# Kernel optimization log

Measured on AMD Instinct MI355X. Metric: run time of the kernel, lower is better.

## Reference

```python
import jax, jax.numpy as jnp
import numpy as np

B, N, C = 8, 3136, 128
NUM_HEADS = 2
HEAD_DIM = C // NUM_HEADS  # 64
SCALE = HEAD_DIM ** -0.5


def setup_inputs() -> dict:
    key = jax.random.key(0)
    ks = jax.random.split(key, 10)
    s = 0.02
    return {
        "x": jax.random.normal(ks[0], (B, N, C), jnp.float32),
        "H": 56,
        "W": 56,
        "relative_pos": jax.random.normal(ks[1], (NUM_HEADS, N, N), jnp.float32),
        "Wq": jax.random.normal(ks[2], (C, C), jnp.float32) * s,
        "bq": jnp.zeros((C,), jnp.float32),
        "Wk": jax.random.normal(ks[3], (C, C), jnp.float32) * s,
        "bk": jnp.zeros((C,), jnp.float32),
        "Wv": jax.random.normal(ks[4], (C, C), jnp.float32) * s,
        "bv": jnp.zeros((C,), jnp.float32),
        "Wp": jax.random.normal(ks[5], (C, C), jnp.float32) * s,
        "bp": jnp.zeros((C,), jnp.float32),
    }


def reference(x, H, W, relative_pos, Wq, bq, Wk, bk, Wv, bv, Wp, bp):
    # x: [B, N, C]; sr_ratio == 1 path of Attention.forward
    b, n, c = x.shape
    h, dh = NUM_HEADS, HEAD_DIM
    # q/k/v projections -> [B, h, N, dh] (torch Linear: x @ W.T + b)
    q = (x @ Wq.T + bq).reshape(b, n, h, dh).transpose(0, 2, 1, 3)
    k = (x @ Wk.T + bk).reshape(b, n, h, dh).transpose(0, 2, 1, 3)
    v = (x @ Wv.T + bv).reshape(b, n, h, dh).transpose(0, 2, 1, 3)
    # scores with additive relative-position bias: [B, h, N, N]
    attn = jnp.einsum("bhnd,bhmd->bhnm", q, k) * SCALE + relative_pos[None]
    attn = jax.nn.softmax(attn, axis=-1)
    # AV -> [B, N, C]
    out = jnp.einsum("bhnm,bhmd->bhnd", attn, v).transpose(0, 2, 1, 3).reshape(b, n, c)
    return out @ Wp.T + bp
```

## Files before the change

### kernel.cpp

```cpp
#include <hip/hip_runtime.h>
#include <hip/hip_fp16.h>

#define N_TOK 3136
#define DH 64
#define NHEAD 2
#define CDIM 128
#define BATCH 8
#define NT 49
#define QK_SCALE 0.18033688011112f
#define LOG2E 1.4426950408889634f

typedef __attribute__((ext_vector_type(8))) short bf16x8;
typedef __attribute__((ext_vector_type(8))) _Float16 f16x8;
typedef __attribute__((ext_vector_type(2))) _Float16 f16x2;
typedef __attribute__((ext_vector_type(2))) __fp16 fp16x2;
typedef __attribute__((ext_vector_type(4))) float f32x4;
typedef __attribute__((ext_vector_type(16))) float f32x16;
typedef __attribute__((ext_vector_type(4))) unsigned short u16x4;
typedef __attribute__((ext_vector_type(4))) unsigned int u32x4;

__device__ __forceinline__ unsigned short f2bf(float f) {
  unsigned int u = __float_as_uint(f);
  u += 0x7fffu + ((u >> 16) & 1u);
  return (unsigned short)(u >> 16);
}

#define MFMA16(a, b, c)    __builtin_amdgcn_mfma_f32_16x16x32_bf16(a, b, c, 0, 0, 0)
#define MFMA32_BF(a, b, c) __builtin_amdgcn_mfma_f32_32x32x16_bf16(a, b, c, 0, 0, 0)
#define MFMA32_F16(a, b, c) __builtin_amdgcn_mfma_f32_32x32x16_f16(a, b, c, 0, 0, 0)

__device__ __forceinline__ void plswap(unsigned& a, unsigned& b) {
  asm volatile("v_permlane32_swap_b32 %0, %1" : "+v"(a), "+v"(b));
}

__device__ __forceinline__ f16x2 pkrtz(float a, float b) {
  union { fp16x2 p; f16x2 h; } cv;
  cv.p = __builtin_amdgcn_cvt_pkrtz(a, b);
  return cv.h;
}

template<bool IN_F32, int OMODE>
__global__ __launch_bounds__(256)
void proj_gemm(const void* __restrict__ Ain, const float* __restrict__ W,
               const float* __restrict__ bias, void* __restrict__ Out,
               float out_scale)
{
  __shared__ __align__(16) unsigned short xs[64][136];
  __shared__ __align__(16) unsigned short wsh[128][136];
  const int tid = threadIdx.x;
  const int m0 = blockIdx.x * 64;
  const int w = tid >> 6, l = tid & 63;
  const int lk = l & 15, lg = l >> 4;

  {
    const float4* Wv = (const float4*)W;
#pragma unroll
    for (int i = 0; i < 16; ++i) {
      int f = tid + i * 256;
      float4 v = Wv[f];
      int row = f >> 5, col = (f & 31) << 2;
      u16x4 pk = { f2bf(v.x), f2bf(v.y), f2bf(v.z), f2bf(v.w) };
      *(u16x4*)&wsh[row][col] = pk;
    }
  }
  if (IN_F32) {
    const float4* Xv = (const float4*)((const float*)Ain + (size_t)m0 * CDIM);
#pragma unroll
    for (int i = 0; i < 8; ++i) {
      int f = tid + i * 256;
      float4 v = Xv[f];
      int row = f >> 5, col = (f & 31) << 2;
      u16x4 pk = { f2bf(v.x), f2bf(v.y), f2bf(v.z), f2bf(v.w) };
      *(u16x4*)&xs[row][col] = pk;
    }
  } else {
    const bf16x8* Xv = (const bf16x8*)((const unsigned short*)Ain + (size_t)m0 * CDIM);
#pragma unroll
    for (int i = 0; i < 4; ++i) {
      int c = tid + i * 256;
      bf16x8 v = Xv[c];
      int row = c >> 4, col = (c & 15) << 3;
      *(bf16x8*)&xs[row][col] = v;
    }
  }
  __syncthreads();

  f32x4 acc[8];
#pragma unroll
  for (int nf = 0; nf < 8; ++nf) acc[nf] = (f32x4){0.f, 0.f, 0.f, 0.f};

#pragma unroll
  for (int kk = 0; kk < 4; ++kk) {
    bf16x8 a = *(const bf16x8*)&xs[w * 16 + lk][kk * 32 + 8 * lg];
#pragma unroll
    for (int nf = 0; nf < 8; ++nf) {
      bf16x8 b = *(const bf16x8*)&wsh[nf * 16 + lk][kk * 32 + 8 * lg];
      acc[nf] = MFMA16(a, b, acc[nf]);
    }
  }

#pragma unroll
  for (int reg = 0; reg < 4; ++reg) {
    int row = m0 + w * 16 + 4 * lg + reg;
    int bb = row / N_TOK;
    int tok = row - bb * N_TOK;
#pragma unroll
    for (int nf = 0; nf < 8; ++nf) {
      int col = nf * 16 + lk;
      float val = (acc[nf][reg] + bias[col]) * out_scale;
      if (OMODE == 0) {
        ((float*)Out)[(size_t)row * CDIM + col] = val;
      } else {
        int head = nf >> 2;
        int d = col & 63;
        size_t idx = ((size_t)(bb * NHEAD + head) * N_TOK + tok) * DH + d;
        if (OMODE == 1) ((unsigned short*)Out)[idx] = f2bf(val);
        else            ((unsigned short*)Out)[idx] = __half_as_ushort(__float2half(val));
      }
    }
  }
}

__global__ __launch_bounds__(256)
void exp_rp(const float* __restrict__ rp, __half* __restrict__ E)
{
  const int hkt = blockIdx.x;
  const int h = hkt / NT, kt = hkt % NT;
  const int q0 = blockIdx.y * 64;
  const int t = threadIdx.x;
  const int kp = t & 63;
  const int qi = t >> 6;

  const int ct = kp >> 5;
  const int kpp = kp & 31;
  const int hi = (kpp >> 2) & 1;
  const int r = (kpp & 3) + ((kpp >> 3) << 2);
  const int didx = hi * 32 + ct * 16 + r;

  const float* src = rp + ((size_t)h * N_TOK + q0) * N_TOK + kt * 64 + kp;
  __half* dst = E + (((size_t)h * NT + kt) * N_TOK + q0) * 64 + didx;

#pragma unroll
  for (int i = 0; i < 16; ++i) {
    int q = qi * 16 + i;
    float v = __expf(src[(size_t)q * N_TOK]);
    dst[(size_t)q * 64] = __float2half(v);
  }
}

__global__ __launch_bounds__(256)
void attn32(const unsigned short* __restrict__ q_ws,
            const unsigned short* __restrict__ k_ws,
            const unsigned short* __restrict__ v_ws,
            const __half* __restrict__ E,
            unsigned short* __restrict__ attn_out)
{
  __shared__ __align__(16) unsigned short LDSU[2][9216];

  const int b = blockIdx.x, qt = blockIdx.y, head = blockIdx.z;
  const int tid = threadIdx.x;
  const int w = tid >> 6, l = tid & 63;
  const int lq = l & 31, hi = l >> 5;

  const size_t bh = ((size_t)b * NHEAD + head) * N_TOK;
  const unsigned short* Kp = k_ws + bh * DH;
  const _Float16* Vg = (const _Float16*)v_ws + bh * DH;

  int qg = qt * 128 + w * 32 + lq;
  if (qg > N_TOK - 1) qg = N_TOK - 1;

  bf16x8 qf[4];
  {
    const unsigned short* qrow = q_ws + (bh + (size_t)qg) * DH + 8 * hi;
#pragma unroll
    for (int ks = 0; ks < 4; ++ks) qf[ks] = *(const bf16x8*)(qrow + 16 * ks);
  }

  const int kr0 = tid >> 3, ku = tid & 7;
  const int kofs = kr0 * 72 + ku * 8;
  const int gk0 = kr0 * DH + ku * 8, gk1 = gk0 + 32 * DH;
  const int vkey = tid & 63;
  const int vd0 = (tid >> 6) << 3;
  const int gv0 = vkey * DH + vd0, gv1 = gv0 + 32;

  const __half* Eb = E + (((size_t)head * NT) * N_TOK + (size_t)qg) * DH + hi * 32;

  float lsum = 0.f;
  f32x16 o0, o1;
#pragma unroll
  for (int i = 0; i < 16; ++i) { o0[i] = 0.f; o1[i] = 0.f; }

  bf16x8 kpreA = *(const bf16x8*)(Kp + gk0);
  bf16x8 kpreB = *(const bf16x8*)(Kp + gk1);
  f16x8 vpreA = *(const f16x8*)(Vg + gv0);
  f16x8 vpreB = *(const f16x8*)(Vg + gv1);

  u32x4 EwA[4], EwB[4];
  {
    const u32x4* ep = (const u32x4*)Eb;
#pragma unroll
    for (int f = 0; f < 4; ++f) EwA[f] = ep[f];
  }

  *(bf16x8*)&LDSU[0][kofs] = kpreA;
  *(bf16x8*)&LDSU[0][kofs + 32 * 72] = kpreB;
#pragma unroll
  for (int j = 0; j < 8; ++j) {
    LDSU[0][4608 + (vd0 + j) * 72 + vkey]      = ((const unsigned short*)&vpreA)[j];
    LDSU[0][4608 + (vd0 + 32 + j) * 72 + vkey] = ((const unsigned short*)&vpreB)[j];
  }
  {
    const unsigned short* kn = Kp + (size_t)64 * DH;
    const _Float16* vn = Vg + (size_t)64 * DH;
    kpreA = *(const bf16x8*)(kn + gk0);
    kpreB = *(const bf16x8*)(kn + gk1);
    vpreA = *(const f16x8*)(vn + gv0);
    vpreB = *(const f16x8*)(vn + gv1);
  }
  asm volatile("s_waitcnt lgkmcnt(0)" ::: "memory");
  __builtin_amdgcn_s_barrier();
  asm volatile("" ::: "memory");

#define ATTN_BODY(PH, KT, EW_CUR, EW_NXT, LAST)                               \
  {                                                                           \
    const unsigned short* Kb = &LDSU[PH][0];                                  \
    const unsigned short* Vb = &LDSU[PH][4608];                               \
    unsigned short* Kn = &LDSU[PH ^ 1][0];                                    \
    unsigned short* Vn = &LDSU[PH ^ 1][4608];                                 \
    if (!(LAST)) {                                         \
      const u32x4* ep = (const u32x4*)(Eb + (size_t)((KT) + 1) * (N_TOK * DH)); \
      _Pragma("unroll") for (int f = 0; f < 4; ++f) EW_NXT[f] = ep[f];        \
    }                                                                         \
                                                           \
    f32x16 s0, s1;                                                            \
    _Pragma("unroll") for (int i = 0; i < 16; ++i) { s0[i] = 0.f; s1[i] = 0.f; } \
    __builtin_amdgcn_s_setprio(1);                                            \
    _Pragma("unroll") for (int ks = 0; ks < 4; ++ks) {                        \
      bf16x8 kf0 = *(const bf16x8*)&Kb[lq * 72 + 16 * ks + 8 * hi];           \
      s0 = MFMA32_BF(kf0, qf[ks], s0);                                        \
      bf16x8 kf1 = *(const bf16x8*)&Kb[(32 + lq) * 72 + 16 * ks + 8 * hi];    \
      s1 = MFMA32_BF(kf1, qf[ks], s1);                                        \
    }                                                                         \
    __builtin_amdgcn_s_setprio(0);                                            \
    if (!(LAST)) {            \
      *(bf16x8*)&Kn[kofs] = kpreA;                                            \
      *(bf16x8*)&Kn[kofs + 32 * 72] = kpreB;                                  \
      _Pragma("unroll") for (int j = 0; j < 8; ++j) {                         \
        Vn[(vd0 + j) * 72 + vkey]      = ((const unsigned short*)&vpreA)[j];  \
        Vn[(vd0 + 32 + j) * 72 + vkey] = ((const unsigned short*)&vpreB)[j];  \
      }                                                                       \
      if ((KT) + 2 < NT) {                                                    \
        const unsigned short* kn2 = Kp + (size_t)((KT) + 2) * 64 * DH;        \
        const _Float16* vn2 = Vg + (size_t)((KT) + 2) * 64 * DH;              \
        kpreA = *(const bf16x8*)(kn2 + gk0);                                  \
        kpreB = *(const bf16x8*)(kn2 + gk1);                                  \
        vpreA = *(const f16x8*)(vn2 + gv0);                                   \
        vpreB = *(const f16x8*)(vn2 + gv1);                                   \
      }                                                                       \
    }                                                                         \
                                \
    unsigned pw[16];                                                          \
    _Pragma("unroll") for (int f = 0; f < 4; ++f) {                           \
      int rb = (f & 1) * 8;                                                   \
      _Pragma("unroll") for (int i = 0; i < 4; ++i) {                         \
        float a = (f >> 1) ? s1[rb + 2 * i] : s0[rb + 2 * i];                 \
        float c = (f >> 1) ? s1[rb + 2 * i + 1] : s0[rb + 2 * i + 1];         \
        f16x2 pp = pkrtz(__builtin_amdgcn_exp2f(a), __builtin_amdgcn_exp2f(c)); \
        union { unsigned u; f16x2 h; } ec; ec.u = EW_CUR[f][i];               \
        f16x2 pr = pp * ec.h;                                                 \
        lsum += (float)pr[0] + (float)pr[1];                                  \
        union { f16x2 h; unsigned u; } pu; pu.h = pr;                         \
        pw[4 * f + i] = pu.u;                                                 \
      }                                                                       \
      plswap(pw[4 * f + 0], pw[4 * f + 2]);                                   \
      plswap(pw[4 * f + 1], pw[4 * f + 3]);                                   \
    }                                                                         \
                                                        \
    __builtin_amdgcn_s_setprio(1);                                            \
    _Pragma("unroll") for (int ks = 0; ks < 4; ++ks) {                        \
      union { unsigned u[4]; f16x8 v; } pf;                                   \
      _Pragma("unroll") for (int i = 0; i < 4; ++i) pf.u[i] = pw[4 * ks + i]; \
      f16x8 vf0 = *(const f16x8*)&Vb[lq * 72 + 16 * ks + 8 * hi];             \
      o0 = MFMA32_F16(vf0, pf.v, o0);                                         \
      f16x8 vf1 = *(const f16x8*)&Vb[(32 + lq) * 72 + 16 * ks + 8 * hi];      \
      o1 = MFMA32_F16(vf1, pf.v, o1);                                         \
    }                                                                         \
    __builtin_amdgcn_s_setprio(0);                                            \
    if (!(LAST)) {                                                            \
      asm volatile("s_waitcnt lgkmcnt(0)" ::: "memory");                      \
      __builtin_amdgcn_s_barrier();                                           \
      asm volatile("" ::: "memory");                                          \
    }                                                                         \
  }

  for (int kt2 = 0; kt2 < (NT - 1) / 2; ++kt2) {
    int kt = 2 * kt2;
    ATTN_BODY(0, kt, EwA, EwB, false);
    ATTN_BODY(1, kt + 1, EwB, EwA, false);
  }
  ATTN_BODY(0, NT - 1, EwA, EwB, true);
#undef ATTN_BODY

  lsum += __shfl_xor(lsum, 32, 64);
  float inv = 1.f / lsum;

  __syncthreads();
  unsigned short* Ot = &LDSU[0][0];
  const int orow = (w * 32 + lq) * 72;
#pragma unroll
  for (int dt = 0; dt < 2; ++dt) {
#pragma unroll
    for (int j = 0; j < 8; ++j) {
      float v0 = (dt ? o1[2 * j] : o0[2 * j]) * inv;
      float v1 = (dt ? o1[2 * j + 1] : o0[2 * j + 1]) * inv;
      unsigned pk;
      asm("v_cvt_pk_bf16_f32 %0, %1, %2" : "=v"(pk) : "v"(v0), "v"(v1));
      int d = ((2 * j) & 3) + 8 * ((2 * j) >> 2) + 4 * hi + 32 * dt;
      *(unsigned*)&Ot[orow + d] = pk;
    }
  }
  __syncthreads();
#pragma unroll
  for (int i = 0; i < 4; ++i) {
    int c = tid + 256 * i;
    int ql = c >> 3, du = c & 7;
    int tok = qt * 128 + ql;
    if (tok < N_TOK) {
      u32x4 val = *(const u32x4*)&Ot[ql * 72 + du * 8];
      *(u32x4*)&attn_out[((size_t)b * N_TOK + tok) * CDIM + head * DH + du * 8] = val;
    }
  }
}

__global__ __launch_bounds__(256)
void attn_fallback(const unsigned short* __restrict__ q_ws,
                   const unsigned short* __restrict__ k_ws,
                   const unsigned short* __restrict__ v_ws,
                   const float* __restrict__ relpos,
                   unsigned short* __restrict__ attn_out)
{
  __shared__ __align__(16) unsigned short Ks[64][72];
  __shared__ __align__(16) unsigned short Vts[64][72];
  __shared__ __align__(16) unsigned short Ps[4][16][72];

  const int b = blockIdx.x, qt = blockIdx.y, head = blockIdx.z;
  const int tid = threadIdx.x;
  const int w = tid >> 6, l = tid & 63;
  const int lk = l & 15, lg = l >> 4;

  const size_t bh = ((size_t)b * NHEAD + head) * N_TOK;
  const unsigned short* Qp = q_ws + (bh + (size_t)qt * 64) * DH;
  const unsigned short* Kp = k_ws + bh * DH;
  const unsigned short* Vg = v_ws + bh * DH;

  bf16x8 qf0, qf1;
  {
    const unsigned short* qrow = Qp + (size_t)(w * 16 + lk) * DH + 8 * lg;
    qf0 = *(const bf16x8*)qrow;
    qf1 = *(const bf16x8*)(qrow + 32);
  }

  const int kr0 = tid >> 3;
  const int ku = (tid & 7) << 3;
  const int gk0 = kr0 * DH + ku;
  const int gk1 = gk0 + 32 * DH;
  const int vkey = tid & 63;
  const int vd0 = (tid >> 6) << 3;
  const int gv0 = vkey * DH + vd0;
  const int gv1 = gv0 + 32;

  const int qrow0 = qt * 64 + w * 16;
  const float* rpb = relpos + (size_t)head * N_TOK * N_TOK +
                     (size_t)(qrow0 + 4 * lg) * N_TOK + lk;

  float l_run[4] = {0.f, 0.f, 0.f, 0.f};
  f32x4 acc[4];
#pragma unroll
  for (int nf = 0; nf < 4; ++nf) acc[nf] = (f32x4){0.f, 0.f, 0.f, 0.f};

  bf16x8 kpreA = *(const bf16x8*)(Kp + gk0);
  bf16x8 kpreB = *(const bf16x8*)(Kp + gk1);
  bf16x8 vpreA = *(const bf16x8*)(Vg + gv0);
  bf16x8 vpreB = *(const bf16x8*)(Vg + gv1);

  for (int kt = 0; kt < NT; ++kt) {
    float rp[4][4];
#pragma unroll
    for (int r = 0; r < 4; ++r)
#pragma unroll
      for (int ct = 0; ct < 4; ++ct)
        rp[ct][r] = rpb[(size_t)r * N_TOK + kt * 64 + ct * 16];

    asm volatile("s_waitcnt lgkmcnt(0)" ::: "memory");
    __builtin_amdgcn_s_barrier();
    asm volatile("" ::: "memory");

    *(bf16x8*)&Ks[kr0][ku] = kpreA;
    *(bf16x8*)&Ks[kr0 + 32][ku] = kpreB;
#pragma unroll
    for (int j = 0; j < 8; ++j) Vts[vd0 + j][vkey] = ((const unsigned short*)&vpreA)[j];
#pragma unroll
    for (int j = 0; j < 8; ++j) Vts[vd0 + 32 + j][vkey] = ((const unsigned short*)&vpreB)[j];

    if (kt + 1 < NT) {
      const unsigned short* kn = Kp + (size_t)(kt + 1) * 64 * DH;
      const unsigned short* vn = Vg + (size_t)(kt + 1) * 64 * DH;
      kpreA = *(const bf16x8*)(kn + gk0);
      kpreB = *(const bf16x8*)(kn + gk1);
      vpreA = *(const bf16x8*)(vn + gv0);
      vpreB = *(const bf16x8*)(vn + gv1);
    }

    asm volatile("s_waitcnt lgkmcnt(0)" ::: "memory");
    __builtin_amdgcn_s_barrier();
    asm volatile("" ::: "memory");

    f32x4 s[4];
#pragma unroll
    for (int ct = 0; ct < 4; ++ct) s[ct] = (f32x4){0.f, 0.f, 0.f, 0.f};
#pragma unroll
    for (int ct = 0; ct < 4; ++ct) {
      bf16x8 kb0 = *(const bf16x8*)&Ks[ct * 16 + lk][8 * lg];
      s[ct] = MFMA16(qf0, kb0, s[ct]);
      bf16x8 kb1 = *(const bf16x8*)&Ks[ct * 16 + lk][32 + 8 * lg];
      s[ct] = MFMA16(qf1, kb1, s[ct]);
    }

#pragma unroll
    for (int ct = 0; ct < 4; ++ct) {
      float p0 = __builtin_amdgcn_exp2f(fmaf(rp[ct][0], LOG2E, s[ct][0]));
      float p1 = __builtin_amdgcn_exp2f(fmaf(rp[ct][1], LOG2E, s[ct][1]));
      float p2 = __builtin_amdgcn_exp2f(fmaf(rp[ct][2], LOG2E, s[ct][2]));
      float p3 = __builtin_amdgcn_exp2f(fmaf(rp[ct][3], LOG2E, s[ct][3]));
      l_run[0] += p0; l_run[1] += p1; l_run[2] += p2; l_run[3] += p3;
      Ps[w][4 * lg + 0][ct * 16 + lk] = f2bf(p0);
      Ps[w][4 * lg + 1][ct * 16 + lk] = f2bf(p1);
      Ps[w][4 * lg + 2][ct * 16 + lk] = f2bf(p2);
      Ps[w][4 * lg + 3][ct * 16 + lk] = f2bf(p3);
    }

    bf16x8 pa0 = *(const bf16x8*)&Ps[w][lk][8 * lg];
    bf16x8 pa1 = *(const bf16x8*)&Ps[w][lk][32 + 8 * lg];
#pragma unroll
    for (int nf = 0; nf < 4; ++nf) {
      bf16x8 vb0 = *(const bf16x8*)&Vts[nf * 16 + lk][8 * lg];
      acc[nf] = MFMA16(pa0, vb0, acc[nf]);
      bf16x8 vb1 = *(const bf16x8*)&Vts[nf * 16 + lk][32 + 8 * lg];
      acc[nf] = MFMA16(pa1, vb1, acc[nf]);
    }
  }

#pragma unroll
  for (int m = 1; m <= 8; m <<= 1)
#pragma unroll
    for (int r = 0; r < 4; ++r)
      l_run[r] += __shfl_xor(l_run[r], m, 64);

#pragma unroll
  for (int r = 0; r < 4; ++r) {
    int tok = qrow0 + 4 * lg + r;
    float inv = 1.f / l_run[r];
#pragma unroll
    for (int nf = 0; nf < 4; ++nf) {
      attn_out[((size_t)b * N_TOK + tok) * CDIM + head * DH + nf * 16 + lk] =
          f2bf(acc[nf][r] * inv);
    }
  }
}

extern "C" void kernel_launch(void* const* d_in, const int* in_sizes, int n_in,
                              void* d_out, int out_size, void* d_ws, size_t ws_size,
                              hipStream_t stream) {
  (void)in_sizes; (void)n_in; (void)out_size;
  const float* x      = (const float*)d_in[0];
  const float* relpos = (const float*)d_in[3];
  const float* Wq = (const float*)d_in[4];  const float* bq = (const float*)d_in[5];
  const float* Wk = (const float*)d_in[6];  const float* bk = (const float*)d_in[7];
  const float* Wv = (const float*)d_in[8];  const float* bv = (const float*)d_in[9];
  const float* Wp = (const float*)d_in[10]; const float* bp = (const float*)d_in[11];

  const size_t QKV_ELEMS = (size_t)BATCH * NHEAD * N_TOK * DH;
  const size_t E_ELEMS   = (size_t)NHEAD * NT * N_TOK * DH;
  unsigned short* q_ws  = (unsigned short*)d_ws;
  unsigned short* k_ws  = q_ws + QKV_ELEMS;
  unsigned short* v_ws  = k_ws + QKV_ELEMS;
  unsigned short* ao_ws = v_ws + QKV_ELEMS;
  __half* E_ws = (__half*)(ao_ws + QKV_ELEMS);

  const bool big = ws_size >= (4 * QKV_ELEMS + E_ELEMS) * sizeof(unsigned short);

  dim3 blk(256);
  const int MTILES = (BATCH * N_TOK) / 64;

  proj_gemm<true, 1><<<MTILES, blk, 0, stream>>>((const void*)x, Wq, bq, (void*)q_ws, QK_SCALE);
  proj_gemm<true, 1><<<MTILES, blk, 0, stream>>>((const void*)x, Wk, bk, (void*)k_ws, 1.f);
  if (big) {
    proj_gemm<true, 2><<<MTILES, blk, 0, stream>>>((const void*)x, Wv, bv, (void*)v_ws, 1.f);
    exp_rp<<<dim3(NHEAD * NT, N_TOK / 64), blk, 0, stream>>>(relpos, E_ws);
    attn32<<<dim3(BATCH, (N_TOK + 127) / 128, NHEAD), blk, 0, stream>>>(
        q_ws, k_ws, v_ws, E_ws, ao_ws);
  } else {
    proj_gemm<true, 1><<<MTILES, blk, 0, stream>>>((const void*)x, Wv, bv, (void*)v_ws, 1.f);
    attn_fallback<<<dim3(BATCH, N_TOK / 64, NHEAD), blk, 0, stream>>>(
        q_ws, k_ws, v_ws, relpos, ao_ws);
  }

  proj_gemm<false, 0><<<MTILES, blk, 0, stream>>>((const void*)ao_ws, Wp, bp, d_out, 1.f);
}
```

Measured before the change: 127.2 us.

## Fuse QKV projections into one kernel and store V transposed for attention

Replaces three separate projection launches with one proj_qkv kernel that loads and converts each x tile once and reuses it for the Q, K and V weight matrices. V is now written in a [d][token] transposed layout, so the attention kernel stages V into LDS with vector stores instead of scattered per-element transposing stores. The row-sum accumulation uses a packed fp16 dot2 instruction. The transposed V store in the projection is strided across tokens, which may make those global writes less coalesced.

```diff
diff --git a/kernel.cpp b/kernel.cpp
--- a/kernel.cpp
+++ b/kernel.cpp
@@ -39,11 +39,52 @@
   return cv.h;
 }
 
-template<bool IN_F32, int OMODE>
+__device__ __forceinline__ float dot2acc(f16x2 pr, float acc) {
+#if __has_builtin(__builtin_amdgcn_fdot2)
+  union { f16x2 h; fp16x2 p; } c; c.h = pr;
+  fp16x2 ones = {(__fp16)1.0f, (__fp16)1.0f};
+  return __builtin_amdgcn_fdot2(c.p, ones, acc, false);
+#else
+  return acc + (float)pr[0] + (float)pr[1];
+#endif
+}
+
+__device__ __forceinline__ void stage_w(const float* __restrict__ W,
+                                        unsigned short (*wsh)[136], int tid) {
+  const float4* Wv4 = (const float4*)W;
+#pragma unroll
+  for (int i = 0; i < 16; ++i) {
+    int f = tid + i * 256;
+    float4 v = Wv4[f];
+    int row = f >> 5, col = (f & 31) << 2;
+    u16x4 pk = { f2bf(v.x), f2bf(v.y), f2bf(v.z), f2bf(v.w) };
+    *(u16x4*)&wsh[row][col] = pk;
+  }
+}
+
+__device__ __forceinline__ void mfma_block(const unsigned short (*xs)[136],
+                                           const unsigned short (*wsh)[136],
+                                           int w, int lk, int lg, f32x4* acc) {
+#pragma unroll
+  for (int nf = 0; nf < 8; ++nf) acc[nf] = (f32x4){0.f, 0.f, 0.f, 0.f};
+#pragma unroll
+  for (int kk = 0; kk < 4; ++kk) {
+    bf16x8 a = *(const bf16x8*)&xs[w * 16 + lk][kk * 32 + 8 * lg];
+#pragma unroll
+    for (int nf = 0; nf < 8; ++nf) {
+      bf16x8 b = *(const bf16x8*)&wsh[nf * 16 + lk][kk * 32 + 8 * lg];
+      acc[nf] = MFMA16(a, b, acc[nf]);
+    }
+  }
+}
+
 __global__ __launch_bounds__(256)
-void proj_gemm(const void* __restrict__ Ain, const float* __restrict__ W,
-               const float* __restrict__ bias, void* __restrict__ Out,
-               float out_scale)
+void proj_qkv(const float* __restrict__ x,
+              const float* __restrict__ Wq, const float* __restrict__ bq,
+              const float* __restrict__ Wk, const float* __restrict__ bk,
+              const float* __restrict__ Wv, const float* __restrict__ bv,
+              unsigned short* __restrict__ qo, unsigned short* __restrict__ ko,
+              unsigned short* __restrict__ vo)
 {
   __shared__ __align__(16) unsigned short xs[64][136];
   __shared__ __align__(16) unsigned short wsh[128][136];
@@ -53,18 +94,7 @@
   const int lk = l & 15, lg = l >> 4;
 
   {
-    const float4* Wv = (const float4*)W;
-#pragma unroll
-    for (int i = 0; i < 16; ++i) {
-      int f = tid + i * 256;
-      float4 v = Wv[f];
-      int row = f >> 5, col = (f & 31) << 2;
-      u16x4 pk = { f2bf(v.x), f2bf(v.y), f2bf(v.z), f2bf(v.w) };
-      *(u16x4*)&wsh[row][col] = pk;
-    }
-  }
-  if (IN_F32) {
-    const float4* Xv = (const float4*)((const float*)Ain + (size_t)m0 * CDIM);
+    const float4* Xv = (const float4*)(x + (size_t)m0 * CDIM);
 #pragma unroll
     for (int i = 0; i < 8; ++i) {
       int f = tid + i * 256;
@@ -73,50 +103,55 @@
       u16x4 pk = { f2bf(v.x), f2bf(v.y), f2bf(v.z), f2bf(v.w) };
       *(u16x4*)&xs[row][col] = pk;
     }
-  } else {
-    const bf16x8* Xv = (const bf16x8*)((const unsigned short*)Ain + (size_t)m0 * CDIM);
-#pragma unroll
-    for (int i = 0; i < 4; ++i) {
-      int c = tid + i * 256;
-      bf16x8 v = Xv[c];
-      int row = c >> 4, col = (c & 15) << 3;
-      *(bf16x8*)&xs[row][col] = v;
-    }
-  }
+  }
+  stage_w(Wq, wsh, tid);
   __syncthreads();
 
   f32x4 acc[8];
-#pragma unroll
-  for (int nf = 0; nf < 8; ++nf) acc[nf] = (f32x4){0.f, 0.f, 0.f, 0.f};
-
-#pragma unroll
-  for (int kk = 0; kk < 4; ++kk) {
-    bf16x8 a = *(const bf16x8*)&xs[w * 16 + lk][kk * 32 + 8 * lg];
-#pragma unroll
-    for (int nf = 0; nf < 8; ++nf) {
-      bf16x8 b = *(const bf16x8*)&wsh[nf * 16 + lk][kk * 32 + 8 * lg];
-      acc[nf] = MFMA16(a, b, acc[nf]);
-    }
-  }
-
+
+  mfma_block(xs, wsh, w, lk, lg, acc);
 #pragma unroll
   for (int reg = 0; reg < 4; ++reg) {
     int row = m0 + w * 16 + 4 * lg + reg;
-    int bb = row / N_TOK;
-    int tok = row - bb * N_TOK;
+    int bb = row / N_TOK, tok = row - bb * N_TOK;
 #pragma unroll
     for (int nf = 0; nf < 8; ++nf) {
       int col = nf * 16 + lk;
-      float val = (acc[nf][reg] + bias[col]) * out_scale;
-      if (OMODE == 0) {
-        ((float*)Out)[(size_t)row * CDIM + col] = val;
-      } else {
-        int head = nf >> 2;
-        int d = col & 63;
-        size_t idx = ((size_t)(bb * NHEAD + head) * N_TOK + tok) * DH + d;
-        if (OMODE == 1) ((unsigned short*)Out)[idx] = f2bf(val);
-        else            ((unsigned short*)Out)[idx] = __half_as_ushort(__float2half(val));
-      }
+      float val = (acc[nf][reg] + bq[col]) * QK_SCALE;
+      qo[((size_t)(bb * NHEAD + (nf >> 2)) * N_TOK + tok) * DH + (col & 63)] = f2bf(val);
+    }
+  }
+  __syncthreads();
+
+  stage_w(Wk, wsh, tid);
+  __syncthreads();
+  mfma_block(xs, wsh, w, lk, lg, acc);
+#pragma unroll
+  for (int reg = 0; reg < 4; ++reg) {
+    int row = m0 + w * 16 + 4 * lg + reg;
+    int bb = row / N_TOK, tok = row - bb * N_TOK;
+#pragma unroll
+    for (int nf = 0; nf < 8; ++nf) {
+      int col = nf * 16 + lk;
+      float val = acc[nf][reg] + bk[col];
+      ko[((size_t)(bb * NHEAD + (nf >> 2)) * N_TOK + tok) * DH + (col & 63)] = f2bf(val);
+    }
+  }
+  __syncthreads();
+
+  stage_w(Wv, wsh, tid);
+  __syncthreads();
+  mfma_block(xs, wsh, w, lk, lg, acc);
+#pragma unroll
+  for (int reg = 0; reg < 4; ++reg) {
+    int row = m0 + w * 16 + 4 * lg + reg;
+    int bb = row / N_TOK, tok = row - bb * N_TOK;
+#pragma unroll
+    for (int nf = 0; nf < 8; ++nf) {
+      int col = nf * 16 + lk;
+      float val = acc[nf][reg] + bv[col];
+      size_t idx = ((size_t)(bb * NHEAD + (nf >> 2)) * DH + (col & 63)) * N_TOK + tok;
+      vo[idx] = __half_as_ushort(__float2half(val));
     }
   }
 }
@@ -164,7 +199,7 @@
 
   const size_t bh = ((size_t)b * NHEAD + head) * N_TOK;
   const unsigned short* Kp = k_ws + bh * DH;
-  const _Float16* Vg = (const _Float16*)v_ws + bh * DH;
+  const _Float16* Vt = (const _Float16*)v_ws + bh * DH;
 
   int qg = qt * 128 + w * 32 + lq;
   if (qg > N_TOK - 1) qg = N_TOK - 1;
@@ -179,9 +214,7 @@
   const int kr0 = tid >> 3, ku = tid & 7;
   const int kofs = kr0 * 72 + ku * 8;
   const int gk0 = kr0 * DH + ku * 8, gk1 = gk0 + 32 * DH;
-  const int vkey = tid & 63;
-  const int vd0 = (tid >> 6) << 3;
-  const int gv0 = vkey * DH + vd0, gv1 = gv0 + 32;
+  const int gvt0 = kr0 * N_TOK + ku * 8, gvt1 = gvt0 + 32 * N_TOK;
 
   const __half* Eb = E + (((size_t)head * NT) * N_TOK + (size_t)qg) * DH + hi * 32;
 
@@ -192,8 +225,8 @@
 
   bf16x8 kpreA = *(const bf16x8*)(Kp + gk0);
   bf16x8 kpreB = *(const bf16x8*)(Kp + gk1);
-  f16x8 vpreA = *(const f16x8*)(Vg + gv0);
-  f16x8 vpreB = *(const f16x8*)(Vg + gv1);
+  f16x8 vpreA = *(const f16x8*)(Vt + gvt0);
+  f16x8 vpreB = *(const f16x8*)(Vt + gvt1);
 
   u32x4 EwA[4], EwB[4];
   {
@@ -204,18 +237,15 @@
 
   *(bf16x8*)&LDSU[0][kofs] = kpreA;
   *(bf16x8*)&LDSU[0][kofs + 32 * 72] = kpreB;
-#pragma unroll
-  for (int j = 0; j < 8; ++j) {
-    LDSU[0][4608 + (vd0 + j) * 72 + vkey]      = ((const unsigned short*)&vpreA)[j];
-    LDSU[0][4608 + (vd0 + 32 + j) * 72 + vkey] = ((const unsigned short*)&vpreB)[j];
-  }
+  *(f16x8*)&LDSU[0][4608 + kofs] = vpreA;
+  *(f16x8*)&LDSU[0][4608 + kofs + 32 * 72] = vpreB;
   {
     const unsigned short* kn = Kp + (size_t)64 * DH;
-    const _Float16* vn = Vg + (size_t)64 * DH;
+    const _Float16* vn = Vt + 64;
     kpreA = *(const bf16x8*)(kn + gk0);
     kpreB = *(const bf16x8*)(kn + gk1);
-    vpreA = *(const f16x8*)(vn + gv0);
-    vpreB = *(const f16x8*)(vn + gv1);
+    vpreA = *(const f16x8*)(vn + gvt0);
+    vpreB = *(const f16x8*)(vn + gvt1);
   }
   asm volatile("s_waitcnt lgkmcnt(0)" ::: "memory");
   __builtin_amdgcn_s_barrier();
@@ -245,17 +275,15 @@
     if (!(LAST)) {            \
       *(bf16x8*)&Kn[kofs] = kpreA;                                            \
       *(bf16x8*)&Kn[kofs + 32 * 72] = kpreB;                                  \
-      _Pragma("unroll") for (int j = 0; j < 8; ++j) {                         \
-        Vn[(vd0 + j) * 72 + vkey]      = ((const unsigned short*)&vpreA)[j];  \
-        Vn[(vd0 + 32 + j) * 72 + vkey] = ((const unsigned short*)&vpreB)[j];  \
-      }                                                                       \
+      *(f16x8*)&Vn[kofs] = vpreA;                                             \
+      *(f16x8*)&Vn[kofs + 32 * 72] = vpreB;                                   \
       if ((KT) + 2 < NT) {                                                    \
         const unsigned short* kn2 = Kp + (size_t)((KT) + 2) * 64 * DH;        \
-        const _Float16* vn2 = Vg + (size_t)((KT) + 2) * 64 * DH;              \
+        const _Float16* vn2 = Vt + (size_t)((KT) + 2) * 64;                   \
         kpreA = *(const bf16x8*)(kn2 + gk0);                                  \
         kpreB = *(const bf16x8*)(kn2 + gk1);                                  \
-        vpreA = *(const f16x8*)(vn2 + gv0);                                   \
-        vpreB = *(const f16x8*)(vn2 + gv1);                                   \
+        vpreA = *(const f16x8*)(vn2 + gvt0);                                  \
+        vpreB = *(const f16x8*)(vn2 + gvt1);                                  \
       }                                                                       \
     }                                                                         \
                                 \
@@ -268,7 +296,7 @@
         f16x2 pp = pkrtz(__builtin_amdgcn_exp2f(a), __builtin_amdgcn_exp2f(c)); \
         union { unsigned u; f16x2 h; } ec; ec.u = EW_CUR[f][i];               \
         f16x2 pr = pp * ec.h;                                                 \
-        lsum += (float)pr[0] + (float)pr[1];                                  \
+        lsum = dot2acc(pr, lsum);                                             \
         union { f16x2 h; unsigned u; } pu; pu.h = pr;                         \
         pw[4 * f + i] = pu.u;                                                 \
       }                                                                       \
@@ -332,6 +360,66 @@
   }
 }
 
+template<bool IN_F32, int OMODE>
+__global__ __launch_bounds__(256)
+void proj_gemm(const void* __restrict__ Ain, const float* __restrict__ W,
+               const float* __restrict__ bias, void* __restrict__ Out,
+               float out_scale)
+{
+  __shared__ __align__(16) unsigned short xs[64][136];
+  __shared__ __align__(16) unsigned short wsh[128][136];
+  const int tid = threadIdx.x;
+  const int m0 = blockIdx.x * 64;
+  const int w = tid >> 6, l = tid & 63;
+  const int lk = l & 15, lg = l >> 4;
+
+  stage_w(W, wsh, tid);
+  if (IN_F32) {
+    const float4* Xv = (const float4*)((const float*)Ain + (size_t)m0 * CDIM);
+#pragma unroll
+    for (int i = 0; i < 8; ++i) {
+      int f = tid + i * 256;
+      float4 v = Xv[f];
+      int row = f >> 5, col = (f & 31) << 2;
+      u16x4 pk = { f2bf(v.x), f2bf(v.y), f2bf(v.z), f2bf(v.w) };
+      *(u16x4*)&xs[row][col] = pk;
+    }
+  } else {
+    const bf16x8* Xv = (const bf16x8*)((const unsigned short*)Ain + (size_t)m0 * CDIM);
+#pragma unroll
+    for (int i = 0; i < 4; ++i) {
+      int c = tid + i * 256;
+      bf16x8 v = Xv[c];
+      int row = c >> 4, col = (c & 15) << 3;
+      *(bf16x8*)&xs[row][col] = v;
+    }
+  }
+  __syncthreads();
+
+  f32x4 acc[8];
+  mfma_block(xs, wsh, w, lk, lg, acc);
+
+#pragma unroll
+  for (int reg = 0; reg < 4; ++reg) {
+    int row = m0 + w * 16 + 4 * lg + reg;
+    int bb = row / N_TOK;
+    int tok = row - bb * N_TOK;
+#pragma unroll
+    for (int nf = 0; nf < 8; ++nf) {
+      int col = nf * 16 + lk;
+      float val = (acc[nf][reg] + bias[col]) * out_scale;
+      if (OMODE == 0) {
+        ((float*)Out)[(size_t)row * CDIM + col] = val;
+      } else {
+        int head = nf >> 2;
+        int d = col & 63;
+        size_t idx = ((size_t)(bb * NHEAD + head) * N_TOK + tok) * DH + d;
+        ((unsigned short*)Out)[idx] = f2bf(val);
+      }
+    }
+  }
+}
+
 __global__ __launch_bounds__(256)
 void attn_fallback(const unsigned short* __restrict__ q_ws,
                    const unsigned short* __restrict__ k_ws,
@@ -492,14 +580,14 @@
   dim3 blk(256);
   const int MTILES = (BATCH * N_TOK) / 64;
 
-  proj_gemm<true, 1><<<MTILES, blk, 0, stream>>>((const void*)x, Wq, bq, (void*)q_ws, QK_SCALE);
-  proj_gemm<true, 1><<<MTILES, blk, 0, stream>>>((const void*)x, Wk, bk, (void*)k_ws, 1.f);
   if (big) {
-    proj_gemm<true, 2><<<MTILES, blk, 0, stream>>>((const void*)x, Wv, bv, (void*)v_ws, 1.f);
+    proj_qkv<<<MTILES, blk, 0, stream>>>(x, Wq, bq, Wk, bk, Wv, bv, q_ws, k_ws, v_ws);
     exp_rp<<<dim3(NHEAD * NT, N_TOK / 64), blk, 0, stream>>>(relpos, E_ws);
     attn32<<<dim3(BATCH, (N_TOK + 127) / 128, NHEAD), blk, 0, stream>>>(
         q_ws, k_ws, v_ws, E_ws, ao_ws);
   } else {
+    proj_gemm<true, 1><<<MTILES, blk, 0, stream>>>((const void*)x, Wq, bq, (void*)q_ws, QK_SCALE);
+    proj_gemm<true, 1><<<MTILES, blk, 0, stream>>>((const void*)x, Wk, bk, (void*)k_ws, 1.f);
     proj_gemm<true, 1><<<MTILES, blk, 0, stream>>>((const void*)x, Wv, bv, (void*)v_ws, 1.f);
     attn_fallback<<<dim3(BATCH, N_TOK / 64, NHEAD), blk, 0, stream>>>(
         q_ws, k_ws, v_ws, relpos, ao_ws);
```

After: 120.9 us. 1.05x faster.
